# Kernel optimization log

Hardware: AMD Instinct MI355X
Metric: run time of the kernel (lower is better)

The kernel has to match this reference:

```python
import jax, jax.numpy as jnp
import numpy as np

N_FM = 100000; N_TP = 4096; N_SM = 100000
IN_FM = 64; IN_SM = 32; IN_TP = 32; IN_GF = 64; HID = 128
E_QOQ = 1000000; E_BP = 1000000; E_CP = 500000; E_CD = 500000; E_RB = 1000000


def setup_inputs():
    key = jax.random.key(0)
    ks = jax.random.split(key, 32)
    rn = lambda k, s, sc=0.05: jax.random.normal(k, s, jnp.float32) * sc
    inp = {}
    inp['x_fm'] = jax.random.normal(ks[0], (N_FM, IN_FM), jnp.float32)
    inp['x_sm'] = jax.random.normal(ks[1], (N_SM, IN_SM), jnp.float32)
    inp['period_vol'] = jax.random.uniform(ks[2], (N_TP, 1), jnp.float32)
    inp['gf'] = jax.random.normal(ks[3], (1, IN_GF), jnp.float32)
    inp['pe_table'] = rn(ks[4], (N_TP, IN_TP), 1.0)  # period_emb weight
    inp['qoq_src'] = jax.random.randint(ks[5], (E_QOQ,), 0, N_FM)
    inp['qoq_dst'] = jax.random.randint(ks[6], (E_QOQ,), 0, N_FM)
    inp['bp_src'] = jax.random.randint(ks[7], (E_BP,), 0, N_FM)
    inp['bp_dst'] = jax.random.randint(ks[8], (E_BP,), 0, N_TP)
    inp['cp_src'] = jax.random.randint(ks[9], (E_CP,), 0, N_TP)
    inp['cp_dst'] = jax.random.randint(ks[10], (E_CP,), 0, N_FM)
    inp['cd_src'] = jax.random.randint(ks[11], (E_CD,), 0, N_TP)
    inp['cd_dst'] = jax.random.randint(ks[12], (E_CD,), 0, N_SM)
    inp['rb_src'] = jax.random.randint(ks[13], (E_RB,), 0, N_TP)
    inp['rb_dst'] = jax.random.randint(ks[14], (E_RB,), 0, N_FM)
    i = 15
    # per-relation SAGEConv params: W_l [in_src,H] + bias, W_r [in_dst,H] (root, no bias)
    for name, ins, ind in [('qoq', IN_FM, IN_FM), ('bp', IN_FM, IN_TP), ('cp', IN_TP, IN_FM), ('cd', IN_TP, IN_SM), ('rb', IN_TP, IN_FM)]:
        inp[name + '_Wl'] = rn(ks[i], (ins, HID)); inp[name + '_bl'] = jnp.zeros((HID,), jnp.float32)
        inp[name + '_Wr'] = rn(ks[i + 1], (ind, HID)); i += 2
    for t in ['fm', 'tp', 'sm']:
        inp['ln_' + t + '_g'] = jnp.ones((HID,), jnp.float32)
        inp['ln_' + t + '_b'] = jnp.zeros((HID,), jnp.float32)
    inp['head_W1'] = rn(ks[i], (HID * 3 + IN_GF, HID // 2)); inp['head_b1'] = jnp.zeros((HID // 2,), jnp.float32)
    inp['head_W2'] = rn(ks[i + 1], (HID // 2, 1)); inp['head_b2'] = jnp.zeros((1,), jnp.float32)
    return inp


def _seg_mean(feat, dst, n):
    s = jax.ops.segment_sum(feat, dst, num_segments=n)
    c = jax.ops.segment_sum(jnp.ones((dst.shape[0], 1), feat.dtype), dst, num_segments=n)
    return s / jnp.maximum(c, 1.0)


def _sage(x_src, x_dst, src, dst, Wl, bl, Wr):
    # PyG SAGEConv: lin_l(mean_j x_j) + lin_r(x_i); aggregate raw features, then transform
    m = _seg_mean(x_src[src], dst, x_dst.shape[0])
    return m @ Wl + bl + x_dst @ Wr


def _ln(x, g, b, eps=1e-5):
    mu = x.mean(-1, keepdims=True)
    xc = x - mu
    var = (xc * xc).mean(-1, keepdims=True)
    return xc / jnp.sqrt(var + eps) * g + b


def _forward(x_fm, x_sm, period_vol, gf, pe_table,
             qoq_Wl, qoq_bl, qoq_Wr, bp_Wl, bp_bl, bp_Wr, cp_Wl, cp_bl, cp_Wr,
             cd_Wl, cd_bl, cd_Wr, rb_Wl, rb_bl, rb_Wr,
             ln_fm_g, ln_fm_b, ln_tp_g, ln_tp_b, ln_sm_g, ln_sm_b,
             head_W1, head_b1, head_W2, head_b2,
             qoq_src, qoq_dst, bp_src, bp_dst, cp_src, cp_dst, cd_src, cd_dst, rb_src, rb_dst):
    pe = pe_table * period_vol  # [T, in_tp]
    # HeteroConv aggr='mean': average relation outputs per destination type
    out_fm = (_sage(x_fm, x_fm, qoq_src, qoq_dst, qoq_Wl, qoq_bl, qoq_Wr)
              + _sage(pe, x_fm, cp_src, cp_dst, cp_Wl, cp_bl, cp_Wr)
              + _sage(pe, x_fm, rb_src, rb_dst, rb_Wl, rb_bl, rb_Wr)) / 3.0
    out_tp = _sage(x_fm, pe, bp_src, bp_dst, bp_Wl, bp_bl, bp_Wr)
    out_sm = _sage(pe, x_sm, cd_src, cd_dst, cd_Wl, cd_bl, cd_Wr)
    fm = jax.nn.relu(_ln(out_fm, ln_fm_g, ln_fm_b))
    tp = jax.nn.relu(_ln(out_tp, ln_tp_g, ln_tp_b))
    sm = jax.nn.relu(_ln(out_sm, ln_sm_g, ln_sm_b))
    h = jnp.concatenate([fm.mean(0), tp.mean(0), sm.mean(0), gf[0]], axis=-1)
    h = jax.nn.relu(h @ head_W1 + head_b1)  # dropout is identity in eval
    return (h @ head_W2 + head_b2).squeeze()


def reference(x_fm, x_sm, period_vol, gf, pe_table,
              qoq_src, qoq_dst, bp_src, bp_dst, cp_src, cp_dst, cd_src, cd_dst, rb_src, rb_dst,
              qoq_Wl, qoq_bl, qoq_Wr, bp_Wl, bp_bl, bp_Wr, cp_Wl, cp_bl, cp_Wr,
              cd_Wl, cd_bl, cd_Wr, rb_Wl, rb_bl, rb_Wr,
              ln_fm_g, ln_fm_b, ln_tp_g, ln_tp_b, ln_sm_g, ln_sm_b,
              head_W1, head_b1, head_W2, head_b2):
    return _forward(x_fm, x_sm, period_vol, gf, pe_table,
                    qoq_Wl, qoq_bl, qoq_Wr, bp_Wl, bp_bl, bp_Wr, cp_Wl, cp_bl, cp_Wr,
                    cd_Wl, cd_bl, cd_Wr, rb_Wl, rb_bl, rb_Wr,
                    ln_fm_g, ln_fm_b, ln_tp_g, ln_tp_b, ln_sm_g, ln_sm_b,
                    head_W1, head_b1, head_W2, head_b2,
                    qoq_src, qoq_dst, bp_src, bp_dst, cp_src, cp_dst, cd_src, cd_dst, rb_src, rb_dst)
```

## Files before the change

### kernel.cpp

```cpp
#include <hip/hip_runtime.h>
#include <hip/hip_fp16.h>

#define N_FM 100000
#define N_TP 4096
#define N_SM 100000
#define HID 128
#define E_QOQ 1000000
#define E_BP 1000000
#define E_CP 500000
#define E_CD 500000
#define E_RB 1000000
#define E_TOT 4000000

#define EO_CP  1000000
#define EO_RB  1500000
#define EO_BP  2500000
#define EO_CD  3500000

#define EL_QOQ 0
#define EL_CP  (N_FM)
#define EL_RB  (2 * N_FM)
#define EL_BP  (3 * N_FM)
#define EL_CD  (3 * N_FM + N_TP)
#define NTOT   (3 * N_FM + N_TP + N_SM)

#define BB_QOQ 0
#define BB_CP  782
#define BB_RB  1173
#define BB_BP  1564
#define BB_CD  1692
#define NBUCK  2083
#define CHUNK  4096
#define NCHUNK ((E_TOT + CHUNK - 1) / CHUNK)

#define PAIRS_CAP 5784064

#define GRID_FM 768
#define GRID_TP 64
#define GRID_SM 1024

__device__ __forceinline__ int bucket_base(int b) {
    if (b < BB_CP) return b * 2048;
    if (b < BB_RB) return 1601536 + (b - BB_CP) * 2048;
    if (b < BB_BP) return 2402304 + (b - BB_RB) * 3584;
    if (b < BB_CD) return 3803648 + (b - BB_BP) * 9216;
    return 4983296 + (b - BB_CD) * 2048;
}

typedef _Float16 h2 __attribute__((ext_vector_type(2)));
typedef _Float16 f16x8_t __attribute__((ext_vector_type(8)));
typedef float f32x4_t __attribute__((ext_vector_type(4)));

union U32H2 { unsigned u; h2 h; };
union U4H8 { uint4 u; f16x8_t h; };

__device__ __forceinline__ unsigned pk2(float a, float b) {
    U32H2 x; x.h = h2{(_Float16)a, (_Float16)b}; return x.u;
}
__device__ __forceinline__ f16x8_t as_h8(uint4 v) { U4H8 x; x.u = v; return x.h; }

#define R1 (N_FM * 32)
#define R2 (R1 + N_SM * 16)
#define R3 (R2 + N_TP * 16)
#define R4 (R3 + 12288)
#define R5 (R4 + 6144)
#define R6 (R5 + 4096)
#define R7 (R6 + 128)

__device__ __forceinline__ unsigned pack_pair(const float* W, int p, int c) {
    return pk2(W[(2 * p) * HID + c], W[(2 * p + 1) * HID + c]);
}

__global__ void pack_all(const float* __restrict__ x_fm, const float* __restrict__ x_sm,
                         const float* __restrict__ pe_table, const float* __restrict__ pvol,
                         const float* __restrict__ qoq_Wl, const float* __restrict__ cp_Wl,
                         const float* __restrict__ rb_Wl, const float* __restrict__ qoq_Wr,
                         const float* __restrict__ cp_Wr, const float* __restrict__ rb_Wr,
                         const float* __restrict__ bp_Wl, const float* __restrict__ bp_Wr,
                         const float* __restrict__ cd_Wl, const float* __restrict__ cd_Wr,
                         const float* __restrict__ qoq_bl, const float* __restrict__ cp_bl,
                         const float* __restrict__ rb_bl,
                         unsigned* __restrict__ x_fm_f, unsigned* __restrict__ x_sm_f,
                         unsigned* __restrict__ pe_f, unsigned* __restrict__ wf_fm,
                         unsigned* __restrict__ wf_tp, unsigned* __restrict__ wf_sm,
                         float* __restrict__ bias_fm) {
    int gid = blockIdx.x * blockDim.x + threadIdx.x;
    if (gid < R1) {
        float2 t = ((const float2*)x_fm)[gid];
        x_fm_f[gid] = pk2(t.x, t.y);
    } else if (gid < R2) {
        int i = gid - R1;
        float2 t = ((const float2*)x_sm)[i];
        x_sm_f[i] = pk2(t.x, t.y);
    } else if (gid < R3) {
        int i = gid - R2;
        float2 t = ((const float2*)pe_table)[i];
        float v = pvol[i >> 4];
        pe_f[i] = pk2(t.x * v, t.y * v);
    } else if (gid < R4) {
        int j = gid - R3;
        int f = j >> 8, lr = (j >> 2) & 63, jj = j & 3;
        int p = (f >> 3) * 16 + ((lr >> 4) << 2) + jj;
        int c = (f & 7) * 16 + (lr & 15);
        unsigned v;
        if (p < 32) v = pack_pair(qoq_Wl, p, c);
        else if (p < 48) v = pack_pair(cp_Wl, p - 32, c);
        else if (p < 64) v = pack_pair(rb_Wl, p - 48, c);
        else {
            int pp = p - 64;
            float u0 = qoq_Wr[(2 * pp) * HID + c] + cp_Wr[(2 * pp) * HID + c] + rb_Wr[(2 * pp) * HID + c];
            float u1 = qoq_Wr[(2 * pp + 1) * HID + c] + cp_Wr[(2 * pp + 1) * HID + c] + rb_Wr[(2 * pp + 1) * HID + c];
            v = pk2(u0, u1);
        }
        wf_fm[j] = v;
    } else if (gid < R5) {
        int j = gid - R4;
        int f = j >> 8, lr = (j >> 2) & 63, jj = j & 3;
        int p = (f >> 3) * 16 + ((lr >> 4) << 2) + jj;
        int c = (f & 7) * 16 + (lr & 15);
        wf_tp[j] = (p < 32) ? pack_pair(bp_Wl, p, c) : pack_pair(bp_Wr, p - 32, c);
    } else if (gid < R6) {
        int j = gid - R5;
        int f = j >> 8, lr = (j >> 2) & 63, jj = j & 3;
        int p = (f >> 3) * 16 + ((lr >> 4) << 2) + jj;
        int c = (f & 7) * 16 + (lr & 15);
        wf_sm[j] = (p < 16) ? pack_pair(cd_Wl, p, c) : pack_pair(cd_Wr, p - 16, c);
    } else if (gid < R7) {
        int c = gid - R6;
        bias_fm[c] = qoq_bl[c] + cp_bl[c] + rb_bl[c];
    }
}

struct EdgePtrs {
    const int *qs, *qd, *cs, *cd_, *rs, *rd, *bs, *bd, *ds, *dd;
};

template <bool NEED_SRC>
__device__ __forceinline__ void edge_decode(const EdgePtrs& P, int e, int& bucket, int& dl, int& src) {
    const int* dp = P.qd; const int* sp = P.qs;
    int i = e, bb = BB_QOQ, sh = 7;
    if (e >= EO_CP) { i = e - EO_CP; dp = P.cd_; sp = P.cs; bb = BB_CP; sh = 8; }
    if (e >= EO_RB) { i = e - EO_RB; dp = P.rd;  sp = P.rs; bb = BB_RB; sh = 8; }
    if (e >= EO_BP) { i = e - EO_BP; dp = P.bd;  sp = P.bs; bb = BB_BP; sh = 5; }
    if (e >= EO_CD) { i = e - EO_CD; dp = P.dd;  sp = P.ds; bb = BB_CD; sh = 8; }
    int d = dp[i];
    bucket = bb + (d >> sh);
    dl = d & ((1 << sh) - 1);
    if (NEED_SRC) src = sp[i];
}

__global__ void __launch_bounds__(256) bin_kernel(EdgePtrs P, int* __restrict__ bwork,
                                                  unsigned* __restrict__ pairs) {
    __shared__ int lh[NBUCK];
    const int tid = threadIdx.x;
    for (int i = tid; i < NBUCK; i += 256) lh[i] = 0;
    __syncthreads();
    const int base = blockIdx.x * CHUNK;
    const int lim = min(base + CHUNK, E_TOT);
    int e = base + tid;
    for (; e + 768 < lim; e += 1024) {
        int b0, b1, b2, b3, dl, s;
        edge_decode<false>(P, e,       b0, dl, s);
        edge_decode<false>(P, e + 256, b1, dl, s);
        edge_decode<false>(P, e + 512, b2, dl, s);
        edge_decode<false>(P, e + 768, b3, dl, s);
        atomicAdd(&lh[b0], 1); atomicAdd(&lh[b1], 1);
        atomicAdd(&lh[b2], 1); atomicAdd(&lh[b3], 1);
    }
    for (; e < lim; e += 256) {
        int b, dl, s;
        edge_decode<false>(P, e, b, dl, s);
        atomicAdd(&lh[b], 1);
    }
    __syncthreads();
#pragma unroll
    for (int u = 0; u < (NBUCK + 255) / 256; u++) {
        int b = tid + u * 256;
        if (b < NBUCK) {
            int c = lh[b];
            lh[b] = c ? bucket_base(b) + atomicAdd(&bwork[b], c) : 0;
        }
    }
    __syncthreads();
    e = base + tid;
    for (; e + 768 < lim; e += 1024) {
        int b0, b1, b2, b3, d0, d1, d2, d3, s0, s1, s2, s3;
        edge_decode<true>(P, e,       b0, d0, s0);
        edge_decode<true>(P, e + 256, b1, d1, s1);
        edge_decode<true>(P, e + 512, b2, d2, s2);
        edge_decode<true>(P, e + 768, b3, d3, s3);
        int p0 = atomicAdd(&lh[b0], 1);
        int p1 = atomicAdd(&lh[b1], 1);
        int p2 = atomicAdd(&lh[b2], 1);
        int p3 = atomicAdd(&lh[b3], 1);
        pairs[p0] = ((unsigned)d0 << 24) | (unsigned)s0;
        pairs[p1] = ((unsigned)d1 << 24) | (unsigned)s1;
        pairs[p2] = ((unsigned)d2 << 24) | (unsigned)s2;
        pairs[p3] = ((unsigned)d3 << 24) | (unsigned)s3;
    }
    for (; e < lim; e += 256) {
        int b, dl, s;
        edge_decode<true>(P, e, b, dl, s);
        int pos = atomicAdd(&lh[b], 1);
        pairs[pos] = ((unsigned)dl << 24) | (unsigned)s;
    }
}

__global__ void __launch_bounds__(256) esort(const int* __restrict__ bwork,
                                             const unsigned* __restrict__ pairs,
                                             int* __restrict__ so,
                                             int* __restrict__ el_beg, int* __restrict__ el_end) {
    __shared__ int hist[256], scn[256];
    const int b = blockIdx.x;
    const int tid = threadIdx.x;
    int beg = bucket_base(b);
    int end = beg + bwork[b];
    int egbase, ne;
    if (b < BB_CP)      { int e0 = (b - BB_QOQ) << 7; egbase = EL_QOQ + e0; ne = min(128, N_FM - e0); }
    else if (b < BB_RB) { int e0 = (b - BB_CP) << 8;  egbase = EL_CP + e0;  ne = min(256, N_FM - e0); }
    else if (b < BB_BP) { int e0 = (b - BB_RB) << 8;  egbase = EL_RB + e0;  ne = min(256, N_FM - e0); }
    else if (b < BB_CD) { int e0 = (b - BB_BP) << 5;  egbase = EL_BP + e0;  ne = min(32, N_TP - e0); }
    else                { int e0 = (b - BB_CD) << 8;  egbase = EL_CD + e0;  ne = min(256, N_SM - e0); }
    hist[tid] = 0;
    __syncthreads();
    for (int e = beg + tid; e < end; e += 256)
        atomicAdd(&hist[pairs[e] >> 24], 1);
    __syncthreads();
    int v = hist[tid];
    scn[tid] = v;
    __syncthreads();
    for (int off = 1; off < 256; off <<= 1) {
        int u = (tid >= off) ? scn[tid - off] : 0;
        __syncthreads();
        scn[tid] += u;
        __syncthreads();
    }
    int excl = scn[tid] - v;
    if (tid < ne) {
        el_beg[egbase + tid] = beg + excl;
        el_end[egbase + tid] = beg + excl + v;
    }
    hist[tid] = excl;
    __syncthreads();
    for (int e = beg + tid; e < end; e += 256) {
        unsigned pr = pairs[e];
        int dl = pr >> 24;
        int pos = atomicAdd(&hist[dl], 1);
        so[beg + pos] = (int)(pr & 0xFFFFFF);
    }
}

template <int LOGP>
__device__ __forceinline__ void gather_one(int g, int lane, const int* __restrict__ begs,
                                           const int* __restrict__ ends,
                                           const int* __restrict__ ssrc,
                                           const unsigned* __restrict__ feat,
                                           unsigned* __restrict__ mean) {
    const int P = 1 << LOGP;
    int beg = begs[g], end = ends[g];
    float alo = 0.0f, ahi = 0.0f;
    int i = beg;
    for (; i + 4 <= end; i += 4) {
        int s0 = ssrc[i], s1 = ssrc[i + 1], s2 = ssrc[i + 2], s3 = ssrc[i + 3];
        unsigned v0 = feat[(size_t)s0 * P + lane];
        unsigned v1 = feat[(size_t)s1 * P + lane];
        unsigned v2 = feat[(size_t)s2 * P + lane];
        unsigned v3 = feat[(size_t)s3 * P + lane];
        U32H2 u;
        u.u = v0; alo += (float)u.h[0]; ahi += (float)u.h[1];
        u.u = v1; alo += (float)u.h[0]; ahi += (float)u.h[1];
        u.u = v2; alo += (float)u.h[0]; ahi += (float)u.h[1];
        u.u = v3; alo += (float)u.h[0]; ahi += (float)u.h[1];
    }
    for (; i < end; i++) {
        unsigned v = feat[(size_t)ssrc[i] * P + lane];
        U32H2 u; u.u = v;
        alo += (float)u.h[0]; ahi += (float)u.h[1];
    }
    float ic = (end > beg) ? 1.0f / (float)(end - beg) : 0.0f;
    mean[(size_t)g * P + lane] = pk2(alo * ic, ahi * ic);
}

#define G1 (N_TP * 32)
#define G2 (G1 + N_FM * 32)
#define G3 (G2 + N_FM * 16)
#define G4 (G3 + N_SM * 16)
#define G5 (G4 + N_FM * 16)

__global__ void gather_all(const int* __restrict__ el_beg, const int* __restrict__ el_end,
                           const int* __restrict__ so_all,
                           const unsigned* __restrict__ x_fm_f, const unsigned* __restrict__ pe_f,
                           unsigned* __restrict__ mean_qoq, unsigned* __restrict__ mean_cp,
                           unsigned* __restrict__ mean_rb, unsigned* __restrict__ mean_bp,
                           unsigned* __restrict__ mean_cd) {
    int gid = blockIdx.x * blockDim.x + threadIdx.x;
    if (gid < G1) {
        gather_one<5>(gid >> 5, gid & 31, el_beg + EL_BP, el_end + EL_BP, so_all, x_fm_f, mean_bp);
    } else if (gid < G2) {
        int i = gid - G1;
        gather_one<5>(i >> 5, i & 31, el_beg + EL_QOQ, el_end + EL_QOQ, so_all, x_fm_f, mean_qoq);
    } else if (gid < G3) {
        int i = gid - G2;
        gather_one<4>(i >> 4, i & 15, el_beg + EL_CP, el_end + EL_CP, so_all, pe_f, mean_cp);
    } else if (gid < G4) {
        int i = gid - G3;
        gather_one<4>(i >> 4, i & 15, el_beg + EL_CD, el_end + EL_CD, so_all, pe_f, mean_cd);
    } else if (gid < G5) {
        int i = gid - G4;
        gather_one<4>(i >> 4, i & 15, el_beg + EL_RB, el_end + EL_RB, so_all, pe_f, mean_rb);
    }
}


__global__ void __launch_bounds__(256)
fm_mfma(const unsigned* __restrict__ mq, const unsigned* __restrict__ mc,
        const unsigned* __restrict__ mr, const unsigned* __restrict__ xf,
        const unsigned* __restrict__ wfrag, const float* __restrict__ bias,
        const float* __restrict__ ln_g, const float* __restrict__ ln_b,
        float* __restrict__ part) {
    __shared__ uint4 wlds[48 * 64];
    const int tid = threadIdx.x, lane = tid & 63, wid = tid >> 6;
    for (int i = tid; i < 48 * 64; i += 256) wlds[i] = ((const uint4*)wfrag)[i];
    const int c0 = lane & 15, ko = lane >> 4;
    float bias_[8], g_[8], b_[8], colacc[8];
#pragma unroll
    for (int nt = 0; nt < 8; nt++) {
        int c = nt * 16 + c0;
        bias_[nt] = bias[c]; g_[nt] = ln_g[c]; b_[nt] = ln_b[c]; colacc[nt] = 0.0f;
    }
    __syncthreads();
    const f32x4_t zero = {0.0f, 0.0f, 0.0f, 0.0f};
    const int ntiles = N_FM / 16;
    for (int tile = blockIdx.x * 4 + wid; tile < ntiles; tile += gridDim.x * 4) {
        const size_t row = (size_t)tile * 16 + c0;
        uint4 av[6];
        av[0] = ((const uint4*)mq)[row * 8 + ko];
        av[1] = ((const uint4*)mq)[row * 8 + 4 + ko];
        av[2] = ((const uint4*)mc)[row * 4 + ko];
        av[3] = ((const uint4*)mr)[row * 4 + ko];
        av[4] = ((const uint4*)xf)[row * 8 + ko];
        av[5] = ((const uint4*)xf)[row * 8 + 4 + ko];
        f32x4_t acc[8];
#pragma unroll
        for (int nt = 0; nt < 8; nt++) acc[nt] = zero;
#pragma unroll
        for (int ks = 0; ks < 6; ks++) {
            f16x8_t af = as_h8(av[ks]);
#pragma unroll
            for (int nt = 0; nt < 8; nt++)
                acc[nt] = __builtin_amdgcn_mfma_f32_16x16x32_f16(
                    af, as_h8(wlds[(ks * 8 + nt) * 64 + lane]), acc[nt], 0, 0, 0);
        }
#pragma unroll
        for (int r = 0; r < 4; r++) {
            float yv[8]; float s = 0.0f, q = 0.0f;
#pragma unroll
            for (int nt = 0; nt < 8; nt++) {
                float y = (acc[nt][r] + bias_[nt]) * (1.0f / 3.0f);
                yv[nt] = y; s += y; q += y * y;
            }
#pragma unroll
            for (int off = 1; off < 16; off <<= 1) { s += __shfl_xor(s, off); q += __shfl_xor(q, off); }
            float mu = s * (1.0f / 128.0f);
            float var = fmaxf(q * (1.0f / 128.0f) - mu * mu, 0.0f);
            float rs = rsqrtf(var + 1e-5f);
#pragma unroll
            for (int nt = 0; nt < 8; nt++)
                colacc[nt] += fmaxf((yv[nt] - mu) * rs * g_[nt] + b_[nt], 0.0f);
        }
    }
#pragma unroll
    for (int nt = 0; nt < 8; nt++) {
        colacc[nt] += __shfl_xor(colacc[nt], 16);
        colacc[nt] += __shfl_xor(colacc[nt], 32);
    }
    __syncthreads();
    float* sred = (float*)wlds;
    if (lane < 16) {
#pragma unroll
        for (int nt = 0; nt < 8; nt++) sred[wid * 128 + nt * 16 + lane] = colacc[nt];
    }
    __syncthreads();
    if (tid < 128)
        part[(size_t)blockIdx.x * 128 + tid] =
            sred[tid] + sred[128 + tid] + sred[256 + tid] + sred[384 + tid];
}

template <int KSA, int KSB>
__global__ void __launch_bounds__(256)
rows_mfma(int ntiles, const unsigned* __restrict__ mA, const unsigned* __restrict__ xB,
          const unsigned* __restrict__ wfrag, const float* __restrict__ bl,
          const float* __restrict__ ln_g, const float* __restrict__ ln_b,
          float* __restrict__ part) {
    constexpr int KS = KSA + KSB;
    __shared__ uint4 wlds[KS * 8 * 64];
    const int tid = threadIdx.x, lane = tid & 63, wid = tid >> 6;
    for (int i = tid; i < KS * 8 * 64; i += 256) wlds[i] = ((const uint4*)wfrag)[i];
    const int c0 = lane & 15, ko = lane >> 4;
    float bias_[8], g_[8], b_[8], colacc[8];
#pragma unroll
    for (int nt = 0; nt < 8; nt++) {
        int c = nt * 16 + c0;
        bias_[nt] = bl[c]; g_[nt] = ln_g[c]; b_[nt] = ln_b[c]; colacc[nt] = 0.0f;
    }
    __syncthreads();
    const f32x4_t zero = {0.0f, 0.0f, 0.0f, 0.0f};
    for (int tile = blockIdx.x * 4 + wid; tile < ntiles; tile += gridDim.x * 4) {
        const size_t row = (size_t)tile * 16 + c0;
        uint4 av[KS];
#pragma unroll
        for (int ks = 0; ks < KSA; ks++) av[ks] = ((const uint4*)mA)[row * (KSA * 4) + ks * 4 + ko];
#pragma unroll
        for (int ks = 0; ks < KSB; ks++) av[KSA + ks] = ((const uint4*)xB)[row * (KSB * 4) + ks * 4 + ko];
        f32x4_t acc[8];
#pragma unroll
        for (int nt = 0; nt < 8; nt++) acc[nt] = zero;
#pragma unroll
        for (int ks = 0; ks < KS; ks++) {
            f16x8_t af = as_h8(av[ks]);
#pragma unroll
            for (int nt = 0; nt < 8; nt++)
                acc[nt] = __builtin_amdgcn_mfma_f32_16x16x32_f16(
                    af, as_h8(wlds[(ks * 8 + nt) * 64 + lane]), acc[nt], 0, 0, 0);
        }
#pragma unroll
        for (int r = 0; r < 4; r++) {
            float yv[8]; float s = 0.0f, q = 0.0f;
#pragma unroll
            for (int nt = 0; nt < 8; nt++) {
                float y = acc[nt][r] + bias_[nt];
                yv[nt] = y; s += y; q += y * y;
            }
#pragma unroll
            for (int off = 1; off < 16; off <<= 1) { s += __shfl_xor(s, off); q += __shfl_xor(q, off); }
            float mu = s * (1.0f / 128.0f);
            float var = fmaxf(q * (1.0f / 128.0f) - mu * mu, 0.0f);
            float rs = rsqrtf(var + 1e-5f);
#pragma unroll
            for (int nt = 0; nt < 8; nt++)
                colacc[nt] += fmaxf((yv[nt] - mu) * rs * g_[nt] + b_[nt], 0.0f);
        }
    }
#pragma unroll
    for (int nt = 0; nt < 8; nt++) {
        colacc[nt] += __shfl_xor(colacc[nt], 16);
        colacc[nt] += __shfl_xor(colacc[nt], 32);
    }
    __syncthreads();
    float* sred = (float*)wlds;
    if (lane < 16) {
#pragma unroll
        for (int nt = 0; nt < 8; nt++) sred[wid * 128 + nt * 16 + lane] = colacc[nt];
    }
    __syncthreads();
    if (tid < 128)
        part[(size_t)blockIdx.x * 128 + tid] =
            sred[tid] + sred[128 + tid] + sred[256 + tid] + sred[384 + tid];
}

__global__ void __launch_bounds__(512)
reduce_cols(const float* __restrict__ part, float* __restrict__ colsum) {
    __shared__ float lds[512];
    const int t = threadIdx.x, col = t & 127, sl = t >> 7;
    int cnt, srcoff, dst;
    if (blockIdx.x == 0)      { cnt = GRID_FM; srcoff = 0;                         dst = 0;   }
    else if (blockIdx.x == 1) { cnt = GRID_TP; srcoff = GRID_FM * 128;             dst = 128; }
    else                      { cnt = GRID_SM; srcoff = (GRID_FM + GRID_TP) * 128; dst = 256; }
    float a = 0.0f;
    for (int i = sl; i < cnt; i += 4) a += part[srcoff + i * 128 + col];
    lds[t] = a;
    __syncthreads();
    if (t < 128) colsum[dst + t] = lds[t] + lds[128 + t] + lds[256 + t] + lds[384 + t];
}

__global__ void head_kernel(const float* __restrict__ colsum, const float* __restrict__ gf,
                            const float* __restrict__ W1, const float* __restrict__ b1,
                            const float* __restrict__ W2, const float* __restrict__ b2,
                            float* __restrict__ out) {
    __shared__ float h[448];
    __shared__ float sh[512];
    __shared__ float h1[64];
    int t = threadIdx.x;
    if (t < 128) h[t] = colsum[t] * (1.0f / N_FM);
    else if (t < 256) h[t] = colsum[t] * (1.0f / N_TP);
    else if (t < 384) h[t] = colsum[t] * (1.0f / N_SM);
    else if (t < 448) h[t] = gf[t - 384];
    __syncthreads();
    {
        int col = t & 63, slice = t >> 6;
        float a = 0.0f;
        for (int k = slice * 56; k < slice * 56 + 56; k++) a += h[k] * W1[k * 64 + col];
        sh[slice * 64 + col] = a;
    }
    __syncthreads();
    if (t < 64) {
        float a = b1[t];
#pragma unroll
        for (int s = 0; s < 8; s++) a += sh[s * 64 + t];
        h1[t] = fmaxf(a, 0.0f);
    }
    __syncthreads();
    if (t < 64) {
        float p = h1[t] * W2[t];
#pragma unroll
        for (int off = 1; off < 64; off <<= 1) p += __shfl_xor(p, off);
        if (t == 0) out[0] = p + b2[0];
    }
}

extern "C" void kernel_launch(void* const* d_in, const int* in_sizes, int n_in,
                              void* d_out, int out_size, void* d_ws, size_t ws_size,
                              hipStream_t stream) {
    const float* x_fm = (const float*)d_in[0];
    const float* x_sm = (const float*)d_in[1];
    const float* period_vol = (const float*)d_in[2];
    const float* gf = (const float*)d_in[3];
    const float* pe_table = (const float*)d_in[4];
    const int* qoq_src = (const int*)d_in[5];
    const int* qoq_dst = (const int*)d_in[6];
    const int* bp_src = (const int*)d_in[7];
    const int* bp_dst = (const int*)d_in[8];
    const int* cp_src = (const int*)d_in[9];
    const int* cp_dst = (const int*)d_in[10];
    const int* cd_src = (const int*)d_in[11];
    const int* cd_dst = (const int*)d_in[12];
    const int* rb_src = (const int*)d_in[13];
    const int* rb_dst = (const int*)d_in[14];
    const float* qoq_Wl = (const float*)d_in[15];
    const float* qoq_bl = (const float*)d_in[16];
    const float* qoq_Wr = (const float*)d_in[17];
    const float* bp_Wl = (const float*)d_in[18];
    const float* bp_bl = (const float*)d_in[19];
    const float* bp_Wr = (const float*)d_in[20];
    const float* cp_Wl = (const float*)d_in[21];
    const float* cp_bl = (const float*)d_in[22];
    const float* cp_Wr = (const float*)d_in[23];
    const float* cd_Wl = (const float*)d_in[24];
    const float* cd_bl = (const float*)d_in[25];
    const float* cd_Wr = (const float*)d_in[26];
    const float* rb_Wl = (const float*)d_in[27];
    const float* rb_bl = (const float*)d_in[28];
    const float* rb_Wr = (const float*)d_in[29];
    const float* ln_fm_g = (const float*)d_in[30];
    const float* ln_fm_b = (const float*)d_in[31];
    const float* ln_tp_g = (const float*)d_in[32];
    const float* ln_tp_b = (const float*)d_in[33];
    const float* ln_sm_g = (const float*)d_in[34];
    const float* ln_sm_b = (const float*)d_in[35];
    const float* head_W1 = (const float*)d_in[36];
    const float* head_b1 = (const float*)d_in[37];
    const float* head_W2 = (const float*)d_in[38];
    const float* head_b2 = (const float*)d_in[39];

    unsigned* wsu = (unsigned*)d_ws;
    size_t off = 0;
    int* bwork = (int*)(wsu + off); off += NBUCK;
    float* colsum = (float*)(wsu + off); off += 384;
    size_t zero_words = off;
    off = (off + 3) & ~(size_t)3;
    unsigned* pairs = wsu + off; off += PAIRS_CAP;
    int* so_all = (int*)(wsu + off); off += PAIRS_CAP;
    int* el_beg = (int*)(wsu + off); off += NTOT;
    int* el_end = (int*)(wsu + off); off += NTOT;
    unsigned* mean_qoq = wsu + off; off += (size_t)N_FM * 32;
    unsigned* mean_cp  = wsu + off; off += (size_t)N_FM * 16;
    unsigned* mean_rb  = wsu + off; off += (size_t)N_FM * 16;
    unsigned* mean_bp  = wsu + off; off += (size_t)N_TP * 32;
    unsigned* mean_cd  = wsu + off; off += (size_t)N_SM * 16;
    unsigned* pe_f     = wsu + off; off += (size_t)N_TP * 16;
    unsigned* x_fm_f   = wsu + off; off += (size_t)N_FM * 32;
    unsigned* x_sm_f   = wsu + off; off += (size_t)N_SM * 16;
    unsigned* wf_fm    = wsu + off; off += 12288;
    unsigned* wf_tp    = wsu + off; off += 6144;
    unsigned* wf_sm    = wsu + off; off += 4096;
    float* bias_fm     = (float*)(wsu + off); off += 128;

    float* part_fm = (float*)pairs;
    float* part_tp = part_fm + GRID_FM * 128;
    float* part_sm = part_tp + GRID_TP * 128;

    hipMemsetAsync(d_ws, 0, zero_words * 4, stream);

    pack_all<<<(R7 + 255) / 256, 256, 0, stream>>>(
        x_fm, x_sm, pe_table, period_vol, qoq_Wl, cp_Wl, rb_Wl, qoq_Wr, cp_Wr, rb_Wr,
        bp_Wl, bp_Wr, cd_Wl, cd_Wr, qoq_bl, cp_bl, rb_bl,
        x_fm_f, x_sm_f, pe_f, wf_fm, wf_tp, wf_sm, bias_fm);

    EdgePtrs EP{qoq_src, qoq_dst, cp_src, cp_dst, rb_src, rb_dst, bp_src, bp_dst, cd_src, cd_dst};

    bin_kernel<<<NCHUNK, 256, 0, stream>>>(EP, bwork, pairs);
    esort<<<NBUCK, 256, 0, stream>>>(bwork, pairs, so_all, el_beg, el_end);
    gather_all<<<(G5 + 255) / 256, 256, 0, stream>>>(el_beg, el_end, so_all, x_fm_f, pe_f,
                                                     mean_qoq, mean_cp, mean_rb, mean_bp, mean_cd);

    fm_mfma<<<GRID_FM, 256, 0, stream>>>(mean_qoq, mean_cp, mean_rb, x_fm_f, wf_fm,
                                         bias_fm, ln_fm_g, ln_fm_b, part_fm);
    rows_mfma<2, 1><<<GRID_TP, 256, 0, stream>>>(N_TP / 16, mean_bp, pe_f, wf_tp,
                                                 bp_bl, ln_tp_g, ln_tp_b, part_tp);
    rows_mfma<1, 1><<<GRID_SM, 256, 0, stream>>>(N_SM / 16, mean_cd, x_sm_f, wf_sm,
                                                 cd_bl, ln_sm_g, ln_sm_b, part_sm);

    reduce_cols<<<3, 512, 0, stream>>>(part_fm, colsum);

    head_kernel<<<1, 512, 0, stream>>>(colsum, gf, head_W1, head_b1, head_W2, head_b2,
                                       (float*)d_out);
}
```

Baseline: 480.3 us.

## Cache decoded edges in registers, stage sort in LDS, widen gather unroll with fdot2

The binning kernel now decodes each edge once, keeps bucket and source in registers between the counting and scatter passes, and no longer reads the edge arrays a second time. The per-bucket sort writes its output into a shared-memory buffer first and then copies it to global memory in contiguous order, which replaces scattered global writes. The gather loop is unrolled to eight loads so more memory requests are in flight, and it accumulates through fdot2 with selector vectors instead of converting each half to float. Costs are higher register and LDS use (about 37 KB per sort block), which may lower occupancy.

```diff
diff --git a/kernel.cpp b/kernel.cpp
--- a/kernel.cpp
+++ b/kernel.cpp
@@ -32,6 +32,7 @@
 #define NBUCK  2083
 #define CHUNK  4096
 #define NCHUNK ((E_TOT + CHUNK - 1) / CHUNK)
+#define EPB    (CHUNK / 256)
 
 #define PAIRS_CAP 5784064
 
@@ -54,10 +55,24 @@
 union U32H2 { unsigned u; h2 h; };
 union U4H8 { uint4 u; f16x8_t h; };
 
+#if defined(__has_builtin)
+#if __has_builtin(__builtin_amdgcn_fdot2)
+#define HAVE_FDOT2 1
+#endif
+#endif
+
 __device__ __forceinline__ unsigned pk2(float a, float b) {
     U32H2 x; x.h = h2{(_Float16)a, (_Float16)b}; return x.u;
 }
 __device__ __forceinline__ f16x8_t as_h8(uint4 v) { U4H8 x; x.u = v; return x.h; }
+
+__device__ __forceinline__ float dot2sel(float acc, h2 v, h2 sel) {
+#ifdef HAVE_FDOT2
+    return __builtin_amdgcn_fdot2(v, sel, acc, false);
+#else
+    return acc + (float)v[0] * (float)sel[0] + (float)v[1] * (float)sel[1];
+#endif
+}
 
 #define R1 (N_FM * 32)
 #define R2 (R1 + N_SM * 16)
@@ -157,20 +172,17 @@
     __syncthreads();
     const int base = blockIdx.x * CHUNK;
     const int lim = min(base + CHUNK, E_TOT);
-    int e = base + tid;
-    for (; e + 768 < lim; e += 1024) {
-        int b0, b1, b2, b3, dl, s;
-        edge_decode<false>(P, e,       b0, dl, s);
-        edge_decode<false>(P, e + 256, b1, dl, s);
-        edge_decode<false>(P, e + 512, b2, dl, s);
-        edge_decode<false>(P, e + 768, b3, dl, s);
-        atomicAdd(&lh[b0], 1); atomicAdd(&lh[b1], 1);
-        atomicAdd(&lh[b2], 1); atomicAdd(&lh[b3], 1);
-    }
-    for (; e < lim; e += 256) {
-        int b, dl, s;
-        edge_decode<false>(P, e, b, dl, s);
-        atomicAdd(&lh[b], 1);
+    unsigned ebd[EPB]; int esr[EPB];
+#pragma unroll
+    for (int j = 0; j < EPB; j++) {
+        int e = base + tid + j * 256;
+        if (e < lim) {
+            int b, dl, s;
+            edge_decode<true>(P, e, b, dl, s);
+            ebd[j] = ((unsigned)b << 8) | (unsigned)dl;
+            esr[j] = s;
+            atomicAdd(&lh[b], 1);
+        }
     }
     __syncthreads();
 #pragma unroll
@@ -182,27 +194,14 @@
         }
     }
     __syncthreads();
-    e = base + tid;
-    for (; e + 768 < lim; e += 1024) {
-        int b0, b1, b2, b3, d0, d1, d2, d3, s0, s1, s2, s3;
-        edge_decode<true>(P, e,       b0, d0, s0);
-        edge_decode<true>(P, e + 256, b1, d1, s1);
-        edge_decode<true>(P, e + 512, b2, d2, s2);
-        edge_decode<true>(P, e + 768, b3, d3, s3);
-        int p0 = atomicAdd(&lh[b0], 1);
-        int p1 = atomicAdd(&lh[b1], 1);
-        int p2 = atomicAdd(&lh[b2], 1);
-        int p3 = atomicAdd(&lh[b3], 1);
-        pairs[p0] = ((unsigned)d0 << 24) | (unsigned)s0;
-        pairs[p1] = ((unsigned)d1 << 24) | (unsigned)s1;
-        pairs[p2] = ((unsigned)d2 << 24) | (unsigned)s2;
-        pairs[p3] = ((unsigned)d3 << 24) | (unsigned)s3;
-    }
-    for (; e < lim; e += 256) {
-        int b, dl, s;
-        edge_decode<true>(P, e, b, dl, s);
-        int pos = atomicAdd(&lh[b], 1);
-        pairs[pos] = ((unsigned)dl << 24) | (unsigned)s;
+#pragma unroll
+    for (int j = 0; j < EPB; j++) {
+        int e = base + tid + j * 256;
+        if (e < lim) {
+            int b = (int)(ebd[j] >> 8);
+            int pos = atomicAdd(&lh[b], 1);
+            pairs[pos] = ((ebd[j] & 255u) << 24) | (unsigned)esr[j];
+        }
     }
 }
 
@@ -211,6 +210,7 @@
                                              int* __restrict__ so,
                                              int* __restrict__ el_beg, int* __restrict__ el_end) {
     __shared__ int hist[256], scn[256];
+    __shared__ int so_lds[9216];
     const int b = blockIdx.x;
     const int tid = threadIdx.x;
     int beg = bucket_base(b);
@@ -246,8 +246,11 @@
         unsigned pr = pairs[e];
         int dl = pr >> 24;
         int pos = atomicAdd(&hist[dl], 1);
-        so[beg + pos] = (int)(pr & 0xFFFFFF);
-    }
+        so_lds[pos] = (int)(pr & 0xFFFFFF);
+    }
+    __syncthreads();
+    const int n = end - beg;
+    for (int i = tid; i < n; i += 256) so[beg + i] = so_lds[i];
 }
 
 template <int LOGP>
@@ -257,25 +260,44 @@
                                            const unsigned* __restrict__ feat,
                                            unsigned* __restrict__ mean) {
     const int P = 1 << LOGP;
+    const h2 SLO = h2{(_Float16)1.0f, (_Float16)0.0f};
+    const h2 SHI = h2{(_Float16)0.0f, (_Float16)1.0f};
     int beg = begs[g], end = ends[g];
     float alo = 0.0f, ahi = 0.0f;
     int i = beg;
-    for (; i + 4 <= end; i += 4) {
-        int s0 = ssrc[i], s1 = ssrc[i + 1], s2 = ssrc[i + 2], s3 = ssrc[i + 3];
+    for (; i + 8 <= end; i += 8) {
+        int s0 = ssrc[i],     s1 = ssrc[i + 1], s2 = ssrc[i + 2], s3 = ssrc[i + 3];
+        int s4 = ssrc[i + 4], s5 = ssrc[i + 5], s6 = ssrc[i + 6], s7 = ssrc[i + 7];
         unsigned v0 = feat[(size_t)s0 * P + lane];
         unsigned v1 = feat[(size_t)s1 * P + lane];
         unsigned v2 = feat[(size_t)s2 * P + lane];
         unsigned v3 = feat[(size_t)s3 * P + lane];
+        unsigned v4 = feat[(size_t)s4 * P + lane];
+        unsigned v5 = feat[(size_t)s5 * P + lane];
+        unsigned v6 = feat[(size_t)s6 * P + lane];
+        unsigned v7 = feat[(size_t)s7 * P + lane];
         U32H2 u;
-        u.u = v0; alo += (float)u.h[0]; ahi += (float)u.h[1];
-        u.u = v1; alo += (float)u.h[0]; ahi += (float)u.h[1];
-        u.u = v2; alo += (float)u.h[0]; ahi += (float)u.h[1];
-        u.u = v3; alo += (float)u.h[0]; ahi += (float)u.h[1];
-    }
-    for (; i < end; i++) {
+        u.u = v0; alo = dot2sel(alo, u.h, SLO); ahi = dot2sel(ahi, u.h, SHI);
+        u.u = v1; alo = dot2sel(alo, u.h, SLO); ahi = dot2sel(ahi, u.h, SHI);
+        u.u = v2; alo = dot2sel(alo, u.h, SLO); ahi = dot2sel(ahi, u.h, SHI);
+        u.u = v3; alo = dot2sel(alo, u.h, SLO); ahi = dot2sel(ahi, u.h, SHI);
+        u.u = v4; alo = dot2sel(alo, u.h, SLO); ahi = dot2sel(ahi, u.h, SHI);
+        u.u = v5; alo = dot2sel(alo, u.h, SLO); ahi = dot2sel(ahi, u.h, SHI);
+        u.u = v6; alo = dot2sel(alo, u.h, SLO); ahi = dot2sel(ahi, u.h, SHI);
+        u.u = v7; alo = dot2sel(alo, u.h, SLO); ahi = dot2sel(ahi, u.h, SHI);
+    }
+    for (; i + 2 <= end; i += 2) {
+        int s0 = ssrc[i], s1 = ssrc[i + 1];
+        unsigned v0 = feat[(size_t)s0 * P + lane];
+        unsigned v1 = feat[(size_t)s1 * P + lane];
+        U32H2 u;
+        u.u = v0; alo = dot2sel(alo, u.h, SLO); ahi = dot2sel(ahi, u.h, SHI);
+        u.u = v1; alo = dot2sel(alo, u.h, SLO); ahi = dot2sel(ahi, u.h, SHI);
+    }
+    if (i < end) {
         unsigned v = feat[(size_t)ssrc[i] * P + lane];
         U32H2 u; u.u = v;
-        alo += (float)u.h[0]; ahi += (float)u.h[1];
+        alo = dot2sel(alo, u.h, SLO); ahi = dot2sel(ahi, u.h, SHI);
     }
     float ic = (end > beg) ? 1.0f / (float)(end - beg) : 0.0f;
     mean[(size_t)g * P + lane] = pk2(alo * ic, ahi * ic);
```

Result: faster. 439.4 us (-8.5%).
